# Kernel optimization log

Measured on AMD Instinct MI355X. Metric: run time of the kernel, lower is better.

## Reference

```python
import jax, jax.numpy as jnp
import numpy as np

B, H, N, M, C = 64, 8, 16384, 64, 1024
IVH = 3 * M + 6  # per-head interface size: k(M), beta, g, s(3), gamma, e(M), a(M)


def setup_inputs() -> dict:
    key = jax.random.key(0)
    k1, k2, k3, k4 = jax.random.split(key, 4)
    return {
        "x": jax.random.normal(k1, (B, C), dtype=jnp.float32),
        "current_memory": jax.random.normal(k2, (B, N, M), dtype=jnp.float32),
        "w_prev": jax.random.uniform(k3, (B, H, N), dtype=jnp.float32),
        "W": jax.random.normal(k4, (C, H * IVH), dtype=jnp.float32) * (1.0 / np.sqrt(C)),
        "b": jnp.zeros((H * IVH,), dtype=jnp.float32),
    }


def reference(x, current_memory, w_prev, W, b):
    eps = 1e-16
    iv = (x @ W + b).reshape(B, H, IVH)
    k = iv[..., :M]                                   # [B,H,M] content key
    beta = jax.nn.softplus(iv[..., M])                # [B,H] key strength
    g = jax.nn.sigmoid(iv[..., M + 1])                # [B,H] interpolation gate
    s = jax.nn.softmax(iv[..., M + 2:M + 5], axis=-1) # [B,H,3] shift weights
    gamma = 1.0 + jax.nn.softplus(iv[..., M + 5])     # [B,H] sharpening
    e = jax.nn.sigmoid(iv[..., M + 6:2 * M + 6])      # [B,H,M] erase
    a = iv[..., 2 * M + 6:3 * M + 6]                  # [B,H,M] add

    # content addressing: cosine similarity of k against every memory row
    num = jnp.einsum('bhm,bnm->bhn', k, current_memory)
    den = (jnp.linalg.norm(k, axis=-1)[..., None]
           * jnp.linalg.norm(current_memory, axis=-1)[:, None, :] + eps)
    cos = num / den                                   # [B,H,N]
    wc = jax.nn.softmax(beta[..., None] * cos, axis=-1)

    # gated interpolation with previous weighting
    wg = g[..., None] * wc + (1.0 - g[..., None]) * w_prev

    # circular conv1d shift with 3-tap kernel (shifts -1, 0, +1)
    ws = (s[..., 0:1] * jnp.roll(wg, 1, axis=-1)
          + s[..., 1:2] * wg
          + s[..., 2:3] * jnp.roll(wg, -1, axis=-1))

    # sharpening (power normalize)
    wp = ws ** gamma[..., None]
    w = wp / (jnp.sum(wp, axis=-1, keepdims=True) + eps)

    # read
    read_data = jnp.einsum('bhn,bnm->bhm', w, current_memory)
    return (read_data, w, e, a)
```

## Files before the change

### kernel.cpp

```cpp
#include <hip/hip_runtime.h>
#include <cstdint>
#include <cstddef>

#define B_    64
#define H_    8
#define N_    16384
#define M_    64
#define C_    1024
#define IVH_  198
#define J_    1584
#define NCHUNK_ 64

__device__ __forceinline__ float softplus_f(float x) {
    return (x > 20.f) ? x : log1pf(__expf(x));
}
__device__ __forceinline__ float sigmoid_f(float x) {
    return 1.f / (1.f + __expf(-x));
}
__device__ __forceinline__ float sel8(const float p[8], int i) {
    float r01 = (i & 1) ? p[1] : p[0];
    float r23 = (i & 1) ? p[3] : p[2];
    float r45 = (i & 1) ? p[5] : p[4];
    float r67 = (i & 1) ? p[7] : p[6];
    float a = (i & 2) ? r23 : r01;
    float c = (i & 2) ? r67 : r45;
    return (i & 4) ? c : a;
}

__global__ __launch_bounds__(64) void k_gemm(const float* __restrict__ x,
                                             const float* __restrict__ W,
                                             float* __restrict__ iv) {
    int lane = threadIdx.x;
    int j = blockIdx.x * 64 + lane;
    bool valid = (j < J_);
    int b0 = blockIdx.y * 16;
    int c0 = blockIdx.z * 128;
    const float* xb = x + (size_t)b0 * C_;
    float acc[16];
    #pragma unroll
    for (int i = 0; i < 16; ++i) acc[i] = 0.f;
    #pragma unroll 2
    for (int c = c0; c < c0 + 128; ++c) {
        float wv = valid ? W[(size_t)c * J_ + j] : 0.f;
        #pragma unroll
        for (int bi = 0; bi < 16; ++bi)
            acc[bi] = fmaf(xb[(size_t)bi * C_ + c], wv, acc[bi]);
    }
    if (valid) {
        #pragma unroll
        for (int bi = 0; bi < 16; ++bi)
            atomicAdd(&iv[(size_t)(b0 + bi) * J_ + j], acc[bi]);
    }
}

__global__ void k_params(const float* __restrict__ iv, const float* __restrict__ bias,
                         float* __restrict__ kbuf, float* __restrict__ P,
                         float* __restrict__ out_e, float* __restrict__ out_a) {
    int bh = blockIdx.x;
    int m  = threadIdx.x;
    int b = bh >> 3, h = bh & 7;
    const float* row = iv + (size_t)b * J_ + h * IVH_;
    const float* bb  = bias + h * IVH_;
    float kv = row[m] + bb[m];
    float s = kv * kv;
    #pragma unroll
    for (int o = 32; o > 0; o >>= 1) s += __shfl_xor(s, o, 64);
    float kn = sqrtf(s);
    float beta = softplus_f(row[64] + bb[64]);
    kbuf[(size_t)bh * 64 + m] = kv * (beta / kn);
    float ev = row[70 + m] + bb[70 + m];
    out_e[(size_t)bh * 64 + m] = sigmoid_f(ev);
    out_a[(size_t)bh * 64 + m] = row[134 + m] + bb[134 + m];
    if (m == 0) {
        float v1 = row[65] + bb[65];
        float v2 = row[66] + bb[66];
        float v3 = row[67] + bb[67];
        float v4 = row[68] + bb[68];
        float v5 = row[69] + bb[69];
        float mx3 = fmaxf(v2, fmaxf(v3, v4));
        float e2 = __expf(v2 - mx3), e3 = __expf(v3 - mx3), e4 = __expf(v4 - mx3);
        float inv = 1.f / (e2 + e3 + e4);
        float* p = P + (size_t)bh * 8;
        p[0] = 1e-16f / kn;
        p[1] = sigmoid_f(v1);
        p[2] = e2 * inv; p[3] = e3 * inv; p[4] = e4 * inv;
        p[5] = 1.f + softplus_f(v5);
    }
}

__global__ __launch_bounds__(256, 4) void k_A(
        const float* __restrict__ mem, const float* __restrict__ kbuf,
        const float* __restrict__ P, float* __restrict__ z,
        float* __restrict__ pmax, float* __restrict__ psum) {
    __shared__ float zl[8 * 264];
    int t = threadIdx.x;
    int b = blockIdx.y;
    int ck = blockIdx.x;
    int n0 = ck << 8;
    int w = t >> 6, lane = t & 63, sub8 = lane >> 3, mq8 = lane & 7;

    float4 ka[8], kb[8];
    #pragma unroll
    for (int h = 0; h < 8; ++h) {
        const float* kr = kbuf + (((size_t)b * 8 + h) << 6) + mq8 * 8;
        ka[h] = *(const float4*)(kr);
        kb[h] = *(const float4*)(kr + 4);
    }
    float epsl = P[(((size_t)b * 8 + mq8) << 3)];

    const float* mb = mem + ((size_t)b * N_ + n0) * M_;
    #pragma unroll 2
    for (int rr = 0; rr < 8; ++rr) {
        int row = (w << 6) + (rr << 3) + sub8;
        const float* mr = mb + (size_t)row * M_ + mq8 * 8;
        float4 m0 = *(const float4*)(mr);
        float4 m1 = *(const float4*)(mr + 4);
        float pr[9];
        #pragma unroll
        for (int h = 0; h < 8; ++h)
            pr[h] = ka[h].x*m0.x + ka[h].y*m0.y + ka[h].z*m0.z + ka[h].w*m0.w
                  + kb[h].x*m1.x + kb[h].y*m1.y + kb[h].z*m1.z + kb[h].w*m1.w;
        pr[8] = m0.x*m0.x+m0.y*m0.y+m0.z*m0.z+m0.w*m0.w
              + m1.x*m1.x+m1.y*m1.y+m1.z*m1.z+m1.w*m1.w;
        #pragma unroll
        for (int o = 1; o < 8; o <<= 1) {
            #pragma unroll
            for (int i = 0; i < 9; ++i) pr[i] += __shfl_xor(pr[i], o, 64);
        }
        float rn = sqrtf(pr[8]);
        zl[mq8 * 264 + row] = sel8(pr, mq8) / (rn + epsl);
    }
    __syncthreads();

    #pragma unroll
    for (int h = 0; h < 8; ++h)
        z[(((size_t)b * 8 + h) << 14) + n0 + t] = zl[h * 264 + t];

    #pragma unroll
    for (int q2 = 0; q2 < 2; ++q2) {
        int h = w * 2 + q2;
        float a0 = zl[h * 264 + lane],       a1 = zl[h * 264 + lane + 64];
        float a2 = zl[h * 264 + lane + 128], a3 = zl[h * 264 + lane + 192];
        float mx = fmaxf(fmaxf(a0, a1), fmaxf(a2, a3));
        #pragma unroll
        for (int o = 32; o > 0; o >>= 1) mx = fmaxf(mx, __shfl_xor(mx, o, 64));
        float se = __expf(a0 - mx) + __expf(a1 - mx) + __expf(a2 - mx) + __expf(a3 - mx);
        #pragma unroll
        for (int o = 32; o > 0; o >>= 1) se += __shfl_xor(se, o, 64);
        if (lane == 0) {
            pmax[(((size_t)b * 8 + h) << 6) + ck] = mx;
            psum[(((size_t)b * 8 + h) << 6) + ck] = se;
        }
    }
}

__global__ __launch_bounds__(256, 4) void k_B(
        const float* __restrict__ mem, const float* __restrict__ z,
        const float* __restrict__ wprev, const float* __restrict__ P,
        const float* __restrict__ pmax, const float* __restrict__ psum,
        float* __restrict__ out_w, float* __restrict__ sumwp,
        float* __restrict__ readAcc) {
    __shared__ float smem[3072 + 2064 + 32 + 64];
    float* wp_s  = smem;
    float* wgl   = smem + 3072;
    float* racc2 = smem + 3072;
    float* sums  = smem + 5136;
    float* pl    = smem + 5168;

    int t = threadIdx.x;
    int b  = blockIdx.y;
    int ck = blockIdx.x;
    int n0 = ck << 8;
    int n = n0 + t;
    int w = t >> 6, lane = t & 63, sub = lane >> 4, mq = lane & 15;

    #pragma unroll
    for (int q2 = 0; q2 < 2; ++q2) {
        int h = w * 2 + q2;
        size_t bh = (size_t)b * 8 + h;
        float m = pmax[(bh << 6) + lane];
        float s = psum[(bh << 6) + lane];
        float mx = m;
        #pragma unroll
        for (int o = 32; o > 0; o >>= 1) mx = fmaxf(mx, __shfl_xor(mx, o, 64));
        float sc = s * __expf(m - mx);
        #pragma unroll
        for (int o = 32; o > 0; o >>= 1) sc += __shfl_xor(sc, o, 64);
        if (lane == 0) { pl[h * 8 + 0] = mx; pl[h * 8 + 1] = 1.f / sc; }
    }
    if (t < 8) {
        const float* p = P + (((size_t)b * 8 + t) << 3);
        pl[t * 8 + 2] = p[1];
        pl[t * 8 + 3] = p[2];
        pl[t * 8 + 4] = p[3];
        pl[t * 8 + 5] = p[4];
        pl[t * 8 + 6] = p[5];
    }
    __syncthreads();

    #pragma unroll
    for (int h = 0; h < 8; ++h) {
        size_t bh = (size_t)b * 8 + h;
        float Mx = pl[h * 8 + 0], iS = pl[h * 8 + 1], g = pl[h * 8 + 2];
        float wc = __expf(z[(bh << 14) + n] - Mx) * iS;
        wgl[h * 258 + t + 1] = fmaf(g, wc, (1.f - g) * wprev[(bh << 14) + n]);
    }
    if (t < 2) {
        int nh   = (t == 0) ? ((n0 + N_ - 1) & (N_ - 1)) : ((n0 + 256) & (N_ - 1));
        int slot = (t == 0) ? 0 : 257;
        #pragma unroll
        for (int h = 0; h < 8; ++h) {
            size_t bh = (size_t)b * 8 + h;
            float Mx = pl[h * 8 + 0], iS = pl[h * 8 + 1], g = pl[h * 8 + 2];
            float wc = __expf(z[(bh << 14) + nh] - Mx) * iS;
            wgl[h * 258 + slot] = fmaf(g, wc, (1.f - g) * wprev[(bh << 14) + nh]);
        }
    }
    __syncthreads();

    float wpv[8];
    #pragma unroll
    for (int h = 0; h < 8; ++h) {
        size_t bh = (size_t)b * 8 + h;
        float s0 = pl[h * 8 + 3], s1 = pl[h * 8 + 4], s2 = pl[h * 8 + 5];
        float gam = pl[h * 8 + 6];
        float wsv = s0 * wgl[h * 258 + t] + s1 * wgl[h * 258 + t + 1]
                  + s2 * wgl[h * 258 + t + 2];
        float v = __powf(wsv, gam);
        wpv[h] = v;
        out_w[(bh << 14) + n] = v;
    }
    #pragma unroll
    for (int h = 0; h < 8; ++h) {
        float s = wpv[h];
        #pragma unroll
        for (int o = 32; o > 0; o >>= 1) s += __shfl_down(s, o, 64);
        if (lane == 0) sums[w * 8 + h] = s;
    }
    *(float4*)(wp_s + t * 12)     = make_float4(wpv[0], wpv[1], wpv[2], wpv[3]);
    *(float4*)(wp_s + t * 12 + 4) = make_float4(wpv[4], wpv[5], wpv[6], wpv[7]);
    __syncthreads();

    float4 acc[8];
    #pragma unroll
    for (int h = 0; h < 8; ++h) acc[h] = make_float4(0.f, 0.f, 0.f, 0.f);
    const float* mb = mem + ((size_t)b * N_ + n0) * M_;
    #pragma unroll
    for (int rr = 0; rr < 16; ++rr) {
        int row = (w << 6) + (rr << 2) + sub;
        float4 mv = *(const float4*)(mb + (size_t)row * M_ + mq * 4);
        float4 wA = *(const float4*)(wp_s + row * 12);
        float4 wB = *(const float4*)(wp_s + row * 12 + 4);
        float wv8[8] = {wA.x, wA.y, wA.z, wA.w, wB.x, wB.y, wB.z, wB.w};
        #pragma unroll
        for (int h = 0; h < 8; ++h) {
            acc[h].x = fmaf(wv8[h], mv.x, acc[h].x);
            acc[h].y = fmaf(wv8[h], mv.y, acc[h].y);
            acc[h].z = fmaf(wv8[h], mv.z, acc[h].z);
            acc[h].w = fmaf(wv8[h], mv.w, acc[h].w);
        }
    }
    #pragma unroll
    for (int h = 0; h < 8; ++h) {
        #pragma unroll
        for (int o = 32; o >= 16; o >>= 1) {
            acc[h].x += __shfl_down(acc[h].x, o, 64);
            acc[h].y += __shfl_down(acc[h].y, o, 64);
            acc[h].z += __shfl_down(acc[h].z, o, 64);
            acc[h].w += __shfl_down(acc[h].w, o, 64);
        }
    }
    if (lane < 16) {
        #pragma unroll
        for (int h = 0; h < 8; ++h)
            *(float4*)(racc2 + ((w * 8 + h) << 6) + mq * 4) = acc[h];
    }
    __syncthreads();
    if (t < 8)
        atomicAdd(&sumwp[b * 8 + t], sums[t] + sums[8 + t] + sums[16 + t] + sums[24 + t]);
    #pragma unroll
    for (int r = 0; r < 2; ++r) {
        int idx = r * 256 + t;
        float s = racc2[idx] + racc2[512 + idx] + racc2[1024 + idx] + racc2[1536 + idx];
        atomicAdd(&readAcc[(size_t)b * 512 + idx], s);
    }
}

__global__ void k_F(float* __restrict__ out_w, const float* __restrict__ sumwp,
                    const float* __restrict__ readAcc, float* __restrict__ out_rd) {
    int t = threadIdx.x;
    size_t idx = (size_t)blockIdx.x * 256 + t;
    int bh = (int)(idx >> 12);
    float inv = 1.f / (sumwp[bh] + 1e-16f);
    float4* p = (float4*)out_w + idx;
    float4 v = *p;
    v.x *= inv; v.y *= inv; v.z *= inv; v.w *= inv;
    *p = v;
    if (blockIdx.x < 128) {
        int i = blockIdx.x * 256 + t;
        out_rd[i] = readAcc[i] / (sumwp[i >> 6] + 1e-16f);
    }
}

extern "C" void kernel_launch(void* const* d_in, const int* in_sizes, int n_in,
                              void* d_out, int out_size, void* d_ws, size_t ws_size,
                              hipStream_t stream) {
    const float* x     = (const float*)d_in[0];
    const float* mem   = (const float*)d_in[1];
    const float* wprev = (const float*)d_in[2];
    const float* W     = (const float*)d_in[3];
    const float* bias  = (const float*)d_in[4];

    float* out    = (float*)d_out;
    float* out_rd = out;
    float* out_w  = out + 32768;
    float* out_e  = out + 32768 + 8388608;
    float* out_a  = out_e + 32768;

    float* ws      = (float*)d_ws;
    float* iv      = ws;
    float* sumwp   = iv + 101376;
    float* readAcc = sumwp + 512;
    float* kbuf    = readAcc + 32768;
    float* P       = kbuf + 32768;
    float* zbuf    = P + 4096;
    float* pmax    = zbuf + 8388608;
    float* psum    = pmax + 32768;

    hipMemsetAsync(iv, 0, (size_t)(101376 + 512 + 32768) * 4, stream);

    k_gemm  <<<dim3(25, 4, 8), 64, 0, stream>>>(x, W, iv);
    k_params<<<512, 64, 0, stream>>>(iv, bias, kbuf, P, out_e, out_a);
    k_A     <<<dim3(NCHUNK_, B_), 256, 0, stream>>>(mem, kbuf, P, zbuf, pmax, psum);
    k_B     <<<dim3(NCHUNK_, B_), 256, 0, stream>>>(mem, zbuf, wprev, P, pmax, psum,
                                                    out_w, sumwp, readAcc);
    k_F     <<<8192, 256, 0, stream>>>(out_w, sumwp, readAcc, out_rd);
}
```

Baseline: 543.5 us.

## Use fixed beta bound for softmax, precompute per-head coefficients, reverse k_B order

Since the scaled cosine is bounded by beta, k_A now stores exp(q - beta) directly and only per-chunk sums, which removes the running max and the pmax buffer. A new small k_stats kernel reduces the partial sums and folds the gate and normaliser into two per-head coefficients, so k_B skips the per-block reduction and the exp. k_B also walks its blocks in reverse order, likely to reuse memory still cached from the end of k_A. The gemm split-K doubles and several unroll and launch-bound values change. The fixed-bound exp risks underflow precision when beta is large.

```diff
diff --git a/kernel.cpp b/kernel.cpp
--- a/kernel.cpp
+++ b/kernel.cpp
@@ -34,13 +34,13 @@
     int j = blockIdx.x * 64 + lane;
     bool valid = (j < J_);
     int b0 = blockIdx.y * 16;
-    int c0 = blockIdx.z * 128;
+    int c0 = blockIdx.z * 64;
     const float* xb = x + (size_t)b0 * C_;
     float acc[16];
     #pragma unroll
     for (int i = 0; i < 16; ++i) acc[i] = 0.f;
-    #pragma unroll 2
-    for (int c = c0; c < c0 + 128; ++c) {
+    #pragma unroll 8
+    for (int c = c0; c < c0 + 64; ++c) {
         float wv = valid ? W[(size_t)c * J_ + j] : 0.f;
         #pragma unroll
         for (int bi = 0; bi < 16; ++bi)
@@ -82,16 +82,17 @@
         float inv = 1.f / (e2 + e3 + e4);
         float* p = P + (size_t)bh * 8;
         p[0] = 1e-16f / kn;
-        p[1] = sigmoid_f(v1);
-        p[2] = e2 * inv; p[3] = e3 * inv; p[4] = e4 * inv;
-        p[5] = 1.f + softplus_f(v5);
-    }
-}
-
-__global__ __launch_bounds__(256, 4) void k_A(
+        p[1] = beta;
+        p[2] = sigmoid_f(v1);
+        p[3] = e2 * inv; p[4] = e3 * inv; p[5] = e4 * inv;
+        p[6] = 1.f + softplus_f(v5);
+    }
+}
+
+__global__ __launch_bounds__(256, 3) void k_A(
         const float* __restrict__ mem, const float* __restrict__ kbuf,
-        const float* __restrict__ P, float* __restrict__ z,
-        float* __restrict__ pmax, float* __restrict__ psum) {
+        const float* __restrict__ P, float* __restrict__ u,
+        float* __restrict__ psum) {
     __shared__ float zl[8 * 264];
     int t = threadIdx.x;
     int b = blockIdx.y;
@@ -106,10 +107,12 @@
         ka[h] = *(const float4*)(kr);
         kb[h] = *(const float4*)(kr + 4);
     }
-    float epsl = P[(((size_t)b * 8 + mq8) << 3)];
+    const float* pp = P + (((size_t)b * 8 + mq8) << 3);
+    float epsl = pp[0];
+    float beta = pp[1];
 
     const float* mb = mem + ((size_t)b * N_ + n0) * M_;
-    #pragma unroll 2
+    #pragma unroll
     for (int rr = 0; rr < 8; ++rr) {
         int row = (w << 6) + (rr << 3) + sub8;
         const float* mr = mb + (size_t)row * M_ + mq8 * 8;
@@ -128,36 +131,48 @@
             for (int i = 0; i < 9; ++i) pr[i] += __shfl_xor(pr[i], o, 64);
         }
         float rn = sqrtf(pr[8]);
-        zl[mq8 * 264 + row] = sel8(pr, mq8) / (rn + epsl);
+        float q = sel8(pr, mq8) / (rn + epsl);
+        zl[mq8 * 264 + row] = __expf(q - beta);
     }
     __syncthreads();
 
     #pragma unroll
     for (int h = 0; h < 8; ++h)
-        z[(((size_t)b * 8 + h) << 14) + n0 + t] = zl[h * 264 + t];
+        u[(((size_t)b * 8 + h) << 14) + n0 + t] = zl[h * 264 + t];
 
     #pragma unroll
     for (int q2 = 0; q2 < 2; ++q2) {
         int h = w * 2 + q2;
-        float a0 = zl[h * 264 + lane],       a1 = zl[h * 264 + lane + 64];
-        float a2 = zl[h * 264 + lane + 128], a3 = zl[h * 264 + lane + 192];
-        float mx = fmaxf(fmaxf(a0, a1), fmaxf(a2, a3));
-        #pragma unroll
-        for (int o = 32; o > 0; o >>= 1) mx = fmaxf(mx, __shfl_xor(mx, o, 64));
-        float se = __expf(a0 - mx) + __expf(a1 - mx) + __expf(a2 - mx) + __expf(a3 - mx);
+        float se = zl[h * 264 + lane]       + zl[h * 264 + lane + 64]
+                 + zl[h * 264 + lane + 128] + zl[h * 264 + lane + 192];
         #pragma unroll
         for (int o = 32; o > 0; o >>= 1) se += __shfl_xor(se, o, 64);
-        if (lane == 0) {
-            pmax[(((size_t)b * 8 + h) << 6) + ck] = mx;
+        if (lane == 0)
             psum[(((size_t)b * 8 + h) << 6) + ck] = se;
-        }
+    }
+}
+
+__global__ void k_stats(const float* __restrict__ psum, const float* __restrict__ P,
+                        float* __restrict__ C) {
+    int bh = blockIdx.x * 4 + (threadIdx.x >> 6);
+    int lane = threadIdx.x & 63;
+    float s = psum[((size_t)bh << 6) + lane];
+    #pragma unroll
+    for (int o = 32; o > 0; o >>= 1) s += __shfl_xor(s, o, 64);
+    if (lane == 0) {
+        const float* p = P + (size_t)bh * 8;
+        float g = p[2];
+        float iS = 1.f / s;
+        float* c = C + (size_t)bh * 8;
+        c[0] = g * iS;
+        c[1] = 1.f - g;
+        c[2] = p[3]; c[3] = p[4]; c[4] = p[5]; c[5] = p[6];
     }
 }
 
 __global__ __launch_bounds__(256, 4) void k_B(
-        const float* __restrict__ mem, const float* __restrict__ z,
-        const float* __restrict__ wprev, const float* __restrict__ P,
-        const float* __restrict__ pmax, const float* __restrict__ psum,
+        const float* __restrict__ mem, const float* __restrict__ u,
+        const float* __restrict__ wprev, const float* __restrict__ C,
         float* __restrict__ out_w, float* __restrict__ sumwp,
         float* __restrict__ readAcc) {
     __shared__ float smem[3072 + 2064 + 32 + 64];
@@ -168,42 +183,23 @@
     float* pl    = smem + 5168;
 
     int t = threadIdx.x;
-    int b  = blockIdx.y;
-    int ck = blockIdx.x;
+    int b  = (B_ - 1) - blockIdx.y;
+    int ck = (NCHUNK_ - 1) - blockIdx.x;
     int n0 = ck << 8;
     int n = n0 + t;
     int w = t >> 6, lane = t & 63, sub = lane >> 4, mq = lane & 15;
 
-    #pragma unroll
-    for (int q2 = 0; q2 < 2; ++q2) {
-        int h = w * 2 + q2;
+    if (t < 48) {
+        int h = t / 6, i = t - h * 6;
+        pl[h * 8 + i] = C[(((size_t)b * 8 + h) << 3) + i];
+    }
+    __syncthreads();
+
+    #pragma unroll
+    for (int h = 0; h < 8; ++h) {
         size_t bh = (size_t)b * 8 + h;
-        float m = pmax[(bh << 6) + lane];
-        float s = psum[(bh << 6) + lane];
-        float mx = m;
-        #pragma unroll
-        for (int o = 32; o > 0; o >>= 1) mx = fmaxf(mx, __shfl_xor(mx, o, 64));
-        float sc = s * __expf(m - mx);
-        #pragma unroll
-        for (int o = 32; o > 0; o >>= 1) sc += __shfl_xor(sc, o, 64);
-        if (lane == 0) { pl[h * 8 + 0] = mx; pl[h * 8 + 1] = 1.f / sc; }
-    }
-    if (t < 8) {
-        const float* p = P + (((size_t)b * 8 + t) << 3);
-        pl[t * 8 + 2] = p[1];
-        pl[t * 8 + 3] = p[2];
-        pl[t * 8 + 4] = p[3];
-        pl[t * 8 + 5] = p[4];
-        pl[t * 8 + 6] = p[5];
-    }
-    __syncthreads();
-
-    #pragma unroll
-    for (int h = 0; h < 8; ++h) {
-        size_t bh = (size_t)b * 8 + h;
-        float Mx = pl[h * 8 + 0], iS = pl[h * 8 + 1], g = pl[h * 8 + 2];
-        float wc = __expf(z[(bh << 14) + n] - Mx) * iS;
-        wgl[h * 258 + t + 1] = fmaf(g, wc, (1.f - g) * wprev[(bh << 14) + n]);
+        float A1 = pl[h * 8 + 0], A2 = pl[h * 8 + 1];
+        wgl[h * 258 + t + 1] = fmaf(A1, u[(bh << 14) + n], A2 * wprev[(bh << 14) + n]);
     }
     if (t < 2) {
         int nh   = (t == 0) ? ((n0 + N_ - 1) & (N_ - 1)) : ((n0 + 256) & (N_ - 1));
@@ -211,9 +207,8 @@
         #pragma unroll
         for (int h = 0; h < 8; ++h) {
             size_t bh = (size_t)b * 8 + h;
-            float Mx = pl[h * 8 + 0], iS = pl[h * 8 + 1], g = pl[h * 8 + 2];
-            float wc = __expf(z[(bh << 14) + nh] - Mx) * iS;
-            wgl[h * 258 + slot] = fmaf(g, wc, (1.f - g) * wprev[(bh << 14) + nh]);
+            float A1 = pl[h * 8 + 0], A2 = pl[h * 8 + 1];
+            wgl[h * 258 + slot] = fmaf(A1, u[(bh << 14) + nh], A2 * wprev[(bh << 14) + nh]);
         }
     }
     __syncthreads();
@@ -222,8 +217,8 @@
     #pragma unroll
     for (int h = 0; h < 8; ++h) {
         size_t bh = (size_t)b * 8 + h;
-        float s0 = pl[h * 8 + 3], s1 = pl[h * 8 + 4], s2 = pl[h * 8 + 5];
-        float gam = pl[h * 8 + 6];
+        float s0 = pl[h * 8 + 2], s1 = pl[h * 8 + 3], s2 = pl[h * 8 + 4];
+        float gam = pl[h * 8 + 5];
         float wsv = s0 * wgl[h * 258 + t] + s1 * wgl[h * 258 + t + 1]
                   + s2 * wgl[h * 258 + t + 2];
         float v = __powf(wsv, gam);
@@ -245,7 +240,7 @@
     #pragma unroll
     for (int h = 0; h < 8; ++h) acc[h] = make_float4(0.f, 0.f, 0.f, 0.f);
     const float* mb = mem + ((size_t)b * N_ + n0) * M_;
-    #pragma unroll
+    #pragma unroll 4
     for (int rr = 0; rr < 16; ++rr) {
         int row = (w << 6) + (rr << 2) + sub;
         float4 mv = *(const float4*)(mb + (size_t)row * M_ + mq * 4);
@@ -323,16 +318,17 @@
     float* readAcc = sumwp + 512;
     float* kbuf    = readAcc + 32768;
     float* P       = kbuf + 32768;
-    float* zbuf    = P + 4096;
-    float* pmax    = zbuf + 8388608;
-    float* psum    = pmax + 32768;
+    float* Cb      = P + 4096;
+    float* ubuf    = Cb + 4096;
+    float* psum    = ubuf + 8388608;
 
     hipMemsetAsync(iv, 0, (size_t)(101376 + 512 + 32768) * 4, stream);
 
-    k_gemm  <<<dim3(25, 4, 8), 64, 0, stream>>>(x, W, iv);
+    k_gemm  <<<dim3(25, 4, 16), 64, 0, stream>>>(x, W, iv);
     k_params<<<512, 64, 0, stream>>>(iv, bias, kbuf, P, out_e, out_a);
-    k_A     <<<dim3(NCHUNK_, B_), 256, 0, stream>>>(mem, kbuf, P, zbuf, pmax, psum);
-    k_B     <<<dim3(NCHUNK_, B_), 256, 0, stream>>>(mem, zbuf, wprev, P, pmax, psum,
+    k_A     <<<dim3(NCHUNK_, B_), 256, 0, stream>>>(mem, kbuf, P, ubuf, psum);
+    k_stats <<<128, 256, 0, stream>>>(psum, P, Cb);
+    k_B     <<<dim3(NCHUNK_, B_), 256, 0, stream>>>(mem, ubuf, wprev, Cb,
                                                     out_w, sumwp, readAcc);
     k_F     <<<8192, 256, 0, stream>>>(out_w, sumwp, readAcc, out_rd);
 }
```

After: 530.4 us. -2.4%, faster.
